# Optimization experiments

Measured on AMD Instinct MI355X. Metric: run time of the kernel, lower is better.

The kernel has to match this reference:

```python
import jax, jax.numpy as jnp
import numpy as np

B, S, H = 32, 512, 768
NHEAD, DH = 8, 96          # 8 heads * 96 = 768
E = 4096                   # edges per sample
NC = 2
NEG = -1e9
EPS = 1e-5


def _p(k, shape, scale=0.02):
    return scale * jax.random.normal(k, shape, dtype=jnp.float32)


def setup_inputs() -> dict:
    key = jax.random.key(0)
    ks = jax.random.split(key, 24)
    z = lambda *s: jnp.zeros(s, jnp.float32)
    return {
        "diff_encoded": jax.random.normal(ks[0], (B, S, H), jnp.float32),
        "msg_encoded": jax.random.normal(ks[1], (B, S, H), jnp.float32),
        "msg_mask": jnp.ones((B, S), jnp.int32),
        "edge_index_diff": jax.random.randint(ks[2], (B, 2, E), 0, S),
        "edge_index_msg": jax.random.randint(ks[3], (B, 2, E), 0, S),
        # GATv2Conv(heads=1): lin_l (source/message), lin_r (target), att vector, output bias
        "gat_wl": _p(ks[4], (H, H)), "gat_bl": z(H),
        "gat_wr": _p(ks[5], (H, H)), "gat_br": z(H),
        "gat_att": _p(ks[6], (H,)), "gat_bias": z(H),
        # cross MultiheadAttention
        "wq": _p(ks[7], (H, H)), "bq": z(H),
        "wk": _p(ks[8], (H, H)), "bk": z(H),
        "wv": _p(ks[9], (H, H)), "bv": z(H),
        "wo": _p(ks[10], (H, H)), "bo": z(H),
        # LayerNorm + MLP head
        "ln_g": jnp.ones((H,), jnp.float32), "ln_b": z(H),
        "fc0_w": _p(ks[11], (H, 512)), "fc0_b": z(512),
        "fc1_w": _p(ks[12], (512, 128)), "fc1_b": z(128),
        "fc2_w": _p(ks[13], (128, NC)), "fc2_b": z(NC),
    }


def _gat_single(x, edges, wl, bl, wr, br, att, bias):
    # GATv2Conv, heads=1, add_self_loops=True. x: [N,H], edges: [2,E] (src, dst).
    N = x.shape[0]
    src, dst = edges[0], edges[1]
    valid = (src < N) & (dst < N)            # clip_edge_index, as a mask
    src = jnp.where(valid, src, 0)
    dst = jnp.where(valid, dst, 0)
    loop = jnp.arange(N, dtype=src.dtype)    # PyG adds self loops
    src_a = jnp.concatenate([src, loop])
    dst_a = jnp.concatenate([dst, loop])
    valid_a = jnp.concatenate([valid, jnp.ones((N,), bool)])
    xl = x @ wl + bl                          # source / message transform
    xr = x @ wr + br                          # target transform
    e = jax.nn.leaky_relu(xl[src_a] + xr[dst_a], 0.2) @ att   # [E+N]
    e = jnp.where(valid_a, e, NEG)
    emax = jax.ops.segment_max(e, dst_a, num_segments=N)
    p = jnp.exp(e - emax[dst_a]) * valid_a.astype(x.dtype)
    denom = jax.ops.segment_sum(p, dst_a, num_segments=N)
    alpha = p / denom[dst_a]
    out = jax.ops.segment_sum(alpha[:, None] * xl[src_a], dst_a, num_segments=N)
    return out + bias


_gat = jax.vmap(_gat_single, in_axes=(0, 0) + (None,) * 6)


def _layernorm(x, g, b):
    mu = jnp.mean(x, -1, keepdims=True)
    var = jnp.mean(jnp.square(x - mu), -1, keepdims=True)
    return (x - mu) * jax.lax.rsqrt(var + EPS) * g + b


def reference(diff_encoded, msg_encoded, msg_mask, edge_index_diff, edge_index_msg,
              gat_wl, gat_bl, gat_wr, gat_br, gat_att, gat_bias,
              wq, bq, wk, bk, wv, bv, wo, bo, ln_g, ln_b,
              fc0_w, fc0_b, fc1_w, fc1_b, fc2_w, fc2_b):
    diff_g = _gat(diff_encoded, edge_index_diff, gat_wl, gat_bl, gat_wr, gat_br, gat_att, gat_bias) + diff_encoded
    msg_g = _gat(msg_encoded, edge_index_msg, gat_wl, gat_bl, gat_wr, gat_br, gat_att, gat_bias) + msg_encoded
    # cross attention: query=diff_g, key/value=msg_g, key_padding_mask = (msg_mask == 0)
    q = (diff_g @ wq + bq).reshape(B, S, NHEAD, DH)
    k = (msg_g @ wk + bk).reshape(B, S, NHEAD, DH)
    v = (msg_g @ wv + bv).reshape(B, S, NHEAD, DH)
    scores = jnp.einsum("bqhd,bkhd->bhqk", q, k) / jnp.sqrt(jnp.float32(DH))
    scores = jnp.where((msg_mask == 0)[:, None, None, :], NEG, scores)
    attn = jax.nn.softmax(scores, axis=-1)
    ctx = jnp.einsum("bhqk,bkhd->bqhd", attn, v).reshape(B, S, H) @ wo + bo
    fused = _layernorm(ctx + diff_g, ln_g, ln_b)
    x = fused[:, 0, :]                                  # CLS token
    x = jax.nn.relu(x @ fc0_w + fc0_b)                  # dropout = identity (eval)
    x = jax.nn.relu(x @ fc1_w + fc1_b)
    return x @ fc2_w + fc2_b
```

## Files before the change

### kernel.cpp

```cpp
#include <hip/hip_runtime.h>
#include <hip/hip_bf16.h>
#include <math.h>

#define BB 32
#define SS 512
#define HH 768
#define NHEADC 8
#define DHC 96
#define EE 4096
#define NCC 2
#define CAPC 128
#define CAP2 32
#define GSL 36
#define XRS 1536
#define NEGV -1000000000.0f
#define EPSV 1e-5f

#define PREP_CVT  12288
#define PREP_WT   2304
#define PREP_BIAS 3
#define PREP_CNT  512
#define PREP_TOT  (PREP_CVT + PREP_WT + PREP_BIAS + PREP_CNT)

typedef __hip_bfloat16 bf16;
typedef __bf16 bf16x8 __attribute__((ext_vector_type(8)));
typedef float f32x4 __attribute__((ext_vector_type(4)));

static __device__ inline unsigned short f2bf_u(float f) {
  __hip_bfloat16 h = __float2bfloat16(f);
  return *(unsigned short*)&h;
}
static __device__ inline float bfu(unsigned short u) {
  return __uint_as_float(((unsigned int)u) << 16);
}
static __device__ inline float bf2f(bf16 h) { return __bfloat162float(h); }

static __device__ inline void gload16(const void* g, void* l) {
  __builtin_amdgcn_global_load_lds(
      (const __attribute__((address_space(1))) void*)g,
      (__attribute__((address_space(3))) void*)l, 16, 0, 0);
}

__global__ __launch_bounds__(256) void k_prep(
    const float* __restrict__ msg_enc, bf16* __restrict__ Abf,
    const float* __restrict__ gat_wl, const float* __restrict__ gat_wr,
    const float* __restrict__ wk, const float* __restrict__ wv,
    bf16* __restrict__ wtA, bf16* __restrict__ wtB,
    const float* __restrict__ gat_bl, const float* __restrict__ gat_br,
    const float* __restrict__ bk, const float* __restrict__ bv,
    float* __restrict__ biasA, float* __restrict__ biasB,
    const int* __restrict__ e_msg, const int* __restrict__ e_diff,
    int* __restrict__ cnt, int* __restrict__ dcnt, int* __restrict__ dsrc)
{
  int blk = blockIdx.x, tid = threadIdx.x;
  if (blk < PREP_CVT) {
    int i = (blk * 256 + tid) * 4;
    float4 v = *(const float4*)(msg_enc + i);
    ushort4 o;
    o.x = f2bf_u(v.x); o.y = f2bf_u(v.y); o.z = f2bf_u(v.z); o.w = f2bf_u(v.w);
    *(ushort4*)((unsigned short*)Abf + i) = o;
    return;
  }
  blk -= PREP_CVT;
  if (blk < PREP_WT) {
    int z = blk / 576, rr = blk - z * 576;
    int bx = rr % 24, by = rr / 24;
    const float* w; bf16* o;
    switch (z) {
      case 0: w = gat_wl; o = wtA; break;
      case 1: w = gat_wr; o = wtA + (size_t)HH * HH; break;
      case 2: w = wk;     o = wtB; break;
      default: w = wv;    o = wtB + (size_t)HH * HH; break;
    }
    __shared__ float t[32][33];
    int n0 = bx * 32, k0 = by * 32;
    int x = tid & 31, y = tid >> 5;
    for (int yy = y; yy < 32; yy += 8)
      t[yy][x] = w[(size_t)(k0 + yy) * HH + n0 + x];
    __syncthreads();
    for (int yy = y; yy < 32; yy += 8)
      o[(size_t)(n0 + yy) * HH + k0 + x] = __float2bfloat16(t[x][yy]);
    return;
  }
  blk -= PREP_WT;
  if (blk < PREP_BIAS) {
    int t = blk * 256 + tid;
    if (t < HH) {
      biasA[t] = gat_bl[t]; biasA[HH + t] = gat_br[t];
      biasB[t] = bk[t];     biasB[HH + t] = bv[t];
    }
    return;
  }
  blk -= PREP_BIAS;
  {
    int i = blk * 256 + tid;
    if (i >= BB * EE) return;
    int b = i / EE, j = i - b * EE;
    int s = e_msg[b * 2 * EE + j], d = e_msg[b * 2 * EE + EE + j];
    if (s >= 0 && s < SS && d >= 0 && d < SS)
      atomicAdd(&cnt[b * SS + d], 1);
    int s2 = e_diff[b * 2 * EE + j], d2 = e_diff[b * 2 * EE + EE + j];
    if (s2 >= 0 && s2 < SS && d2 == 0) {
      int pos = atomicAdd(&dcnt[b], 1);
      if (pos < CAPC) dsrc[b * CAPC + pos] = s2;
    }
    if (j == 0) {
      int pos = atomicAdd(&dcnt[b], 1);
      if (pos < CAPC) dsrc[b * CAPC + pos] = 0;
    }
  }
}

template <typename OT>
__global__ __launch_bounds__(256) void k_gemm(
    const bf16* __restrict__ A, const bf16* __restrict__ Bt,
    const float* __restrict__ bias, OT* __restrict__ C,
    int M, int N, int K, int ldc)
{
  __shared__ __align__(16) bf16 As0[128 * 32];
  __shared__ __align__(16) bf16 As1[128 * 32];
  __shared__ __align__(16) bf16 Bs0[128 * 32];
  __shared__ __align__(16) bf16 Bs1[128 * 32];
  const int tid = threadIdx.x;
  const int wv = tid >> 6, lane = tid & 63;
  const int bm = blockIdx.x * 128, bn = blockIdx.y * 128;
  const int wm = (wv & 1) * 64, wn = (wv >> 1) * 64;
  const int m16 = lane & 15, half = lane >> 4;
  f32x4 acc[4][4];
  #pragma unroll
  for (int i = 0; i < 4; ++i)
    #pragma unroll
    for (int j = 0; j < 4; ++j) acc[i][j] = (f32x4){0.f, 0.f, 0.f, 0.f};

  const int c0 = tid, c1 = tid + 256;
  const int r0 = c0 >> 2, o0 = (c0 & 3) * 8;
  const int r1 = c1 >> 2, o1 = (c1 & 3) * 8;
  const size_t aB0 = (size_t)(bm + r0) * K + o0;
  const size_t aB1 = (size_t)(bm + r1) * K + o1;
  const size_t bB0 = (size_t)(bn + r0) * K + o0;
  const size_t bB1 = (size_t)(bn + r1) * K + o1;

  for (int k0 = 0; k0 < K; k0 += 64) {
    __syncthreads();
    gload16(A + aB0 + k0, As0 + (size_t)c0 * 8);
    gload16(A + aB1 + k0, As0 + (size_t)c1 * 8);
    gload16(A + aB0 + k0 + 32, As1 + (size_t)c0 * 8);
    gload16(A + aB1 + k0 + 32, As1 + (size_t)c1 * 8);
    gload16(Bt + bB0 + k0, Bs0 + (size_t)c0 * 8);
    gload16(Bt + bB1 + k0, Bs0 + (size_t)c1 * 8);
    gload16(Bt + bB0 + k0 + 32, Bs1 + (size_t)c0 * 8);
    gload16(Bt + bB1 + k0 + 32, Bs1 + (size_t)c1 * 8);
    __syncthreads();
    #pragma unroll
    for (int ks = 0; ks < 2; ++ks) {
      const bf16* Ah = ks ? As1 : As0;
      const bf16* Bh = ks ? Bs1 : Bs0;
      bf16x8 af[4], bfv[4];
      #pragma unroll
      for (int t = 0; t < 4; ++t) {
        af[t]  = *(const bf16x8*)(Ah + (wm + t * 16 + m16) * 32 + half * 8);
        bfv[t] = *(const bf16x8*)(Bh + (wn + t * 16 + m16) * 32 + half * 8);
      }
      #pragma unroll
      for (int i = 0; i < 4; ++i)
        #pragma unroll
        for (int j = 0; j < 4; ++j)
          acc[i][j] = __builtin_amdgcn_mfma_f32_16x16x32_bf16(af[i], bfv[j], acc[i][j], 0, 0, 0);
    }
  }
  #pragma unroll
  for (int i = 0; i < 4; ++i) {
    #pragma unroll
    for (int j = 0; j < 4; ++j) {
      int col = bn + wn + j * 16 + m16;
      float bv = bias ? bias[col] : 0.f;
      #pragma unroll
      for (int r = 0; r < 4; ++r) {
        int row = bm + wm + i * 16 + half * 4 + r;
        float v = acc[i][j][r] + bv;
        if constexpr (sizeof(OT) == 2)
          C[(size_t)row * ldc + col] = (OT)__float2bfloat16(v);
        else
          C[(size_t)row * ldc + col] = v;
      }
    }
  }
}

__global__ __launch_bounds__(512) void k_scan(const int* __restrict__ cnt,
                                              int* __restrict__ offs,
                                              int* __restrict__ cursor) {
  __shared__ int tmp[SS];
  int b = blockIdx.x, t = threadIdx.x;
  int x = cnt[b * SS + t];
  tmp[t] = x;
  __syncthreads();
  for (int off = 1; off < SS; off <<= 1) {
    int u = (t >= off) ? tmp[t - off] : 0;
    __syncthreads();
    tmp[t] += u;
    __syncthreads();
  }
  int ex = tmp[t] - x;
  offs[b * SS + t] = ex;
  cursor[b * SS + t] = ex;
}

__global__ void k_scatter(const int* __restrict__ e_msg, int* __restrict__ cursor,
                          int* __restrict__ binned) {
  int i = blockIdx.x * blockDim.x + threadIdx.x;
  if (i >= BB * EE) return;
  int b = i / EE, j = i - b * EE;
  int s = e_msg[b * 2 * EE + j], d = e_msg[b * 2 * EE + EE + j];
  if (s >= 0 && s < SS && d >= 0 && d < SS) {
    int pos = atomicAdd(&cursor[b * SS + d], 1);
    binned[(size_t)b * EE + pos] = s;
  }
}

__global__ __launch_bounds__(256) void k_gat_fused(
    const int* __restrict__ binned, const int* __restrict__ offs,
    const int* __restrict__ cnt, const bf16* __restrict__ xlr,
    const float* __restrict__ att, const float* __restrict__ gbias,
    const float* __restrict__ resid, bf16* __restrict__ out)
{
  int g = blockIdx.x * 4 + (threadIdx.x >> 6);
  int lane = threadIdx.x & 63;
  int b = g / SS, d = g - b * SS;
  int base = offs[b * SS + d], n = cnt[b * SS + d];
  const int* bin = binned + (size_t)b * EE + base;
  float av[12];
  {
    const float4* a4 = (const float4*)att;
    #pragma unroll
    for (int r = 0; r < 3; ++r) {
      float4 t = a4[lane + 64 * r];
      av[4*r] = t.x; av[4*r+1] = t.y; av[4*r+2] = t.z; av[4*r+3] = t.w;
    }
  }
  float xr[12];
  {
    const ushort4* p = (const ushort4*)(xlr + ((size_t)b * SS + d) * XRS + HH);
    #pragma unroll
    for (int r = 0; r < 3; ++r) {
      ushort4 v = p[lane + 64 * r];
      xr[4*r] = bfu(v.x); xr[4*r+1] = bfu(v.y); xr[4*r+2] = bfu(v.z); xr[4*r+3] = bfu(v.w);
    }
  }
  float m = -3.0e38f, l = 0.f;
  float acc[12] = {};
  for (int i = -1; i < n; ++i) {
    int s = (i < 0) ? d : bin[i];
    float xs[12];
    const ushort4* p = (const ushort4*)(xlr + ((size_t)b * SS + s) * XRS);
    #pragma unroll
    for (int r = 0; r < 3; ++r) {
      ushort4 v = p[lane + 64 * r];
      xs[4*r] = bfu(v.x); xs[4*r+1] = bfu(v.y); xs[4*r+2] = bfu(v.z); xs[4*r+3] = bfu(v.w);
    }
    float e = 0.f;
    #pragma unroll
    for (int k = 0; k < 12; ++k) {
      float t = xs[k] + xr[k];
      t = t > 0.f ? t : 0.2f * t;
      e += t * av[k];
    }
    #pragma unroll
    for (int off = 32; off > 0; off >>= 1) e += __shfl_xor(e, off);
    float mn = fmaxf(m, e);
    float so = __expf(m - mn);
    float w  = __expf(e - mn);
    l = l * so + w;
    #pragma unroll
    for (int k = 0; k < 12; ++k) acc[k] = acc[k] * so + w * xs[k];
    m = mn;
  }
  float inv = 1.f / l;
  size_t o = ((size_t)b * SS + d) * HH;
  const float4* gb4 = (const float4*)gbias;
  const float4* rs4 = (const float4*)(resid + o);
  ushort4* out4 = (ushort4*)(out + o);
  #pragma unroll
  for (int r = 0; r < 3; ++r) {
    int c = lane + 64 * r;
    float4 gg = gb4[c], rr = rs4[c];
    ushort4 ov;
    ov.x = f2bf_u(acc[4*r+0] * inv + gg.x + rr.x);
    ov.y = f2bf_u(acc[4*r+1] * inv + gg.y + rr.y);
    ov.z = f2bf_u(acc[4*r+2] * inv + gg.z + rr.z);
    ov.w = f2bf_u(acc[4*r+3] * inv + gg.w + rr.w);
    out4[c] = ov;
  }
}

__global__ __launch_bounds__(192) void k_gather_diff(
    const int* __restrict__ dcnt, const int* __restrict__ dsrc,
    const float* __restrict__ diff_enc, bf16* __restrict__ G)
{
  int b = blockIdx.y, jj = blockIdx.x;
  int n = min(dcnt[b], CAP2);
  int t = threadIdx.x;
  size_t orow = ((size_t)b * GSL + jj) * HH;
  ushort4 o = {0, 0, 0, 0};
  if (jj < n || jj == CAP2) {
    int s = (jj == CAP2) ? 0 : dsrc[b * CAPC + jj];
    float4 v = ((const float4*)(diff_enc + ((size_t)b * SS + s) * HH))[t];
    o.x = f2bf_u(v.x); o.y = f2bf_u(v.y); o.z = f2bf_u(v.z); o.w = f2bf_u(v.w);
  }
  *(ushort4*)((unsigned short*)G + orow + t * 4) = o;
}

__global__ __launch_bounds__(256) void k_diff_gat0(
    const int* __restrict__ dcnt, const float* __restrict__ GD,
    const float* __restrict__ att, const float* __restrict__ gbias,
    const float* __restrict__ diff_enc, float* __restrict__ dg0)
{
  int b = blockIdx.x;
  int n = min(dcnt[b], CAP2);
  __shared__ float ee[CAP2];
  __shared__ float al[CAP2];
  __shared__ float xr0s[HH];
  int wave = threadIdx.x >> 6, lane = threadIdx.x & 63;
  for (int h = threadIdx.x; h < HH; h += 256)
    xr0s[h] = GD[((size_t)b * GSL + CAP2) * XRS + HH + h];
  __syncthreads();
  for (int jj = wave; jj < n; jj += 4) {
    const float* px = GD + ((size_t)b * GSL + jj) * XRS;
    float part = 0.f;
    #pragma unroll
    for (int r = 0; r < HH / 64; ++r) {
      int h = lane + 64 * r;
      float t = px[h] + xr0s[h];
      t = t > 0.f ? t : 0.2f * t;
      part += t * att[h];
    }
    #pragma unroll
    for (int off = 32; off > 0; off >>= 1) part += __shfl_xor(part, off);
    if (lane == 0) ee[jj] = part;
  }
  __syncthreads();
  if (threadIdx.x == 0) {
    float m = -3.0e38f;
    for (int i = 0; i < n; ++i) m = fmaxf(m, ee[i]);
    float ssum = 0.f;
    for (int i = 0; i < n; ++i) ssum += expf(ee[i] - m);
    float inv = 1.f / ssum;
    for (int i = 0; i < n; ++i) al[i] = expf(ee[i] - m) * inv;
  }
  __syncthreads();
  for (int h = threadIdx.x; h < HH; h += 256) {
    float acc = 0.f;
    for (int i = 0; i < n; ++i) acc += al[i] * GD[((size_t)b * GSL + i) * XRS + h];
    dg0[b * HH + h] = acc + gbias[h] + diff_enc[(size_t)b * SS * HH + h];
  }
}

__global__ __launch_bounds__(256) void k_colmat(
    const float* __restrict__ in, const float* __restrict__ w,
    const float* __restrict__ bias, const float* __restrict__ extra,
    float* __restrict__ outp, int Kd, int Nd, long in_stride, int relu)
{
  int b = blockIdx.y, n0 = blockIdx.x * 64;
  int tid = threadIdx.x, wv = tid >> 6, lane = tid & 63;
  __shared__ float xs[HH];
  __shared__ float red[4][64];
  const float* src = in + (size_t)b * in_stride;
  for (int k = tid; k < Kd; k += 256) xs[k] = src[k];
  __syncthreads();
  int h = n0 + lane;
  int kpw = Kd >> 2;
  int kb = wv * kpw;
  float acc = 0.f;
  for (int k = 0; k < kpw; k += 8) {
    #pragma unroll
    for (int u = 0; u < 8; ++u) {
      int kk = kb + k + u;
      acc += xs[kk] * w[(size_t)kk * Nd + h];
    }
  }
  red[wv][lane] = acc;
  __syncthreads();
  if (tid < 64) {
    float s = red[0][tid] + red[1][tid] + red[2][tid] + red[3][tid] + bias[n0 + tid];
    if (extra) s += extra[(size_t)b * Nd + n0 + tid];
    if (relu) s = fmaxf(s, 0.f);
    outp[(size_t)b * Nd + n0 + tid] = s;
  }
}

__global__ __launch_bounds__(256) void k_ln(
    const float* __restrict__ xin, const float* __restrict__ g,
    const float* __restrict__ bta, float* __restrict__ yout)
{
  int b = blockIdx.x, tid = threadIdx.x;
  __shared__ float red[4], redq[4];
  float v0 = xin[b * HH + tid];
  float v1 = xin[b * HH + tid + 256];
  float v2 = xin[b * HH + tid + 512];
  float sum = v0 + v1 + v2;
  float sq = v0 * v0 + v1 * v1 + v2 * v2;
  #pragma unroll
  for (int off = 32; off > 0; off >>= 1) { sum += __shfl_xor(sum, off); sq += __shfl_xor(sq, off); }
  int wv = tid >> 6, lane = tid & 63;
  if (lane == 0) { red[wv] = sum; redq[wv] = sq; }
  __syncthreads();
  sum = red[0] + red[1] + red[2] + red[3];
  sq = redq[0] + redq[1] + redq[2] + redq[3];
  float mu = sum / HH;
  float var = sq / HH - mu * mu;
  float scl = rsqrtf(var + EPSV);
  yout[b * HH + tid]       = (v0 - mu) * scl * g[tid]       + bta[tid];
  yout[b * HH + tid + 256] = (v1 - mu) * scl * g[tid + 256] + bta[tid + 256];
  yout[b * HH + tid + 512] = (v2 - mu) * scl * g[tid + 512] + bta[tid + 512];
}

__global__ __launch_bounds__(256) void k_fc12(
    const float* __restrict__ a0g, const float* __restrict__ fc1w,
    const float* __restrict__ fc1b, const float* __restrict__ fc2w,
    const float* __restrict__ fc2b, float* __restrict__ out)
{
  int b = blockIdx.x, tid = threadIdx.x;
  __shared__ float a0s[512];
  __shared__ float a1s[128];
  __shared__ float r1[2][128];
  for (int k = tid; k < 512; k += 256) a0s[k] = a0g[b * 512 + k];
  __syncthreads();
  int o = tid & 127, hf = tid >> 7;
  int kb = hf * 256;
  float acc = 0.f;
  for (int k = 0; k < 256; k += 8) {
    #pragma unroll
    for (int u = 0; u < 8; ++u) {
      int kk = kb + k + u;
      acc += a0s[kk] * fc1w[(size_t)kk * 128 + o];
    }
  }
  r1[hf][o] = acc;
  __syncthreads();
  if (tid < 128) a1s[tid] = fmaxf(r1[0][tid] + r1[1][tid] + fc1b[tid], 0.f);
  __syncthreads();
  if (tid < 128) {
    int oo = tid >> 6, l = tid & 63;
    float p = a1s[l] * fc2w[l * 2 + oo] + a1s[l + 64] * fc2w[(l + 64) * 2 + oo];
    #pragma unroll
    for (int off = 32; off > 0; off >>= 1) p += __shfl_xor(p, off);
    if (l == 0) out[b * NCC + oo] = p + fc2b[oo];
  }
}

__global__ __launch_bounds__(512) void k_attn(
    const float* __restrict__ q0, const bf16* __restrict__ kvb,
    const int* __restrict__ mask, float* __restrict__ ctx)
{
  int b = blockIdx.x / NHEADC, hd = blockIdx.x % NHEADC;
  __shared__ float qs[DHC];
  __shared__ float sc[SS];
  __shared__ float redm[8];
  __shared__ float reds[8];
  __shared__ float pr4[4][DHC];
  int tid = threadIdx.x;
  if (tid < DHC) qs[tid] = q0[b * HH + hd * DHC + tid];
  __syncthreads();
  const float scale = 0.10206207261596575f;
  {
    int s = tid;
    const int4* pk4 = (const int4*)(kvb + ((size_t)b * SS + s) * XRS + hd * DHC);
    float acc = 0.f;
    #pragma unroll
    for (int c = 0; c < 12; ++c) {
      int4 raw = pk4[c];
      const unsigned short* u = (const unsigned short*)&raw;
      #pragma unroll
      for (int j = 0; j < 8; ++j) acc += qs[c * 8 + j] * bfu(u[j]);
    }
    sc[s] = (mask[b * SS + s] != 0) ? acc * scale : NEGV;
  }
  __syncthreads();
  int wave = tid >> 6, lane = tid & 63;
  float m = sc[tid];
  #pragma unroll
  for (int off = 32; off > 0; off >>= 1) m = fmaxf(m, __shfl_xor(m, off));
  if (lane == 0) redm[wave] = m;
  __syncthreads();
  m = redm[0];
  #pragma unroll
  for (int i = 1; i < 8; ++i) m = fmaxf(m, redm[i]);
  float p0 = expf(sc[tid] - m);
  float ssum = p0;
  #pragma unroll
  for (int off = 32; off > 0; off >>= 1) ssum += __shfl_xor(ssum, off);
  if (lane == 0) reds[wave] = ssum;
  __syncthreads();
  ssum = reds[0] + reds[1] + reds[2] + reds[3] + reds[4] + reds[5] + reds[6] + reds[7];
  float inv = 1.f / ssum;
  sc[tid] = p0 * inv;
  __syncthreads();
  {
    int hs = tid >> 7, d = tid & 127;
    if (d < DHC) {
      const bf16* pv = kvb + ((size_t)b * SS + hs * 128) * XRS + HH + hd * DHC + d;
      float acc = 0.f;
      for (int s = 0; s < 128; s += 8) {
        #pragma unroll
        for (int u = 0; u < 8; ++u)
          acc += sc[hs * 128 + s + u] * bf2f(pv[(size_t)(s + u) * XRS]);
      }
      pr4[hs][d] = acc;
    }
  }
  __syncthreads();
  if (tid < DHC)
    ctx[b * HH + hd * DHC + tid] = pr4[0][tid] + pr4[1][tid] + pr4[2][tid] + pr4[3][tid];
}

extern "C" void kernel_launch(void* const* d_in, const int* in_sizes, int n_in,
                              void* d_out, int out_size, void* d_ws, size_t ws_size,
                              hipStream_t stream) {
  const float* diff_enc = (const float*)d_in[0];
  const float* msg_enc  = (const float*)d_in[1];
  const int*   msg_mask = (const int*)d_in[2];
  const int*   e_diff   = (const int*)d_in[3];
  const int*   e_msg    = (const int*)d_in[4];
  const float* gat_wl   = (const float*)d_in[5];
  const float* gat_bl   = (const float*)d_in[6];
  const float* gat_wr   = (const float*)d_in[7];
  const float* gat_br   = (const float*)d_in[8];
  const float* gat_att  = (const float*)d_in[9];
  const float* gat_bias = (const float*)d_in[10];
  const float* wq = (const float*)d_in[11];
  const float* bq = (const float*)d_in[12];
  const float* wk = (const float*)d_in[13];
  const float* bk = (const float*)d_in[14];
  const float* wv = (const float*)d_in[15];
  const float* bv = (const float*)d_in[16];
  const float* wo = (const float*)d_in[17];
  const float* bo = (const float*)d_in[18];
  const float* ln_g = (const float*)d_in[19];
  const float* ln_b = (const float*)d_in[20];
  const float* fc0w = (const float*)d_in[21];
  const float* fc0b = (const float*)d_in[22];
  const float* fc1w = (const float*)d_in[23];
  const float* fc1b = (const float*)d_in[24];
  const float* fc2w = (const float*)d_in[25];
  const float* fc2b = (const float*)d_in[26];
  float* out = (float*)d_out;

  char* ws = (char*)d_ws;
  size_t off = 0;
  auto alloc = [&](size_t bytes) -> void* {
    void* p = (void*)(ws + off);
    off += (bytes + 255) & ~(size_t)255;
    return p;
  };
  bf16* Abf    = (bf16*)alloc((size_t)BB * SS * HH * 2);
  bf16* xlr    = (bf16*)alloc((size_t)BB * SS * XRS * 2);
  bf16* kv     = (bf16*)alloc((size_t)BB * SS * XRS * 2);
  bf16* mg     = (bf16*)alloc((size_t)BB * SS * HH * 2);
  bf16* wtA    = (bf16*)alloc((size_t)2 * HH * HH * 2);
  bf16* wtB    = (bf16*)alloc((size_t)2 * HH * HH * 2);
  float* biasA = (float*)alloc((size_t)XRS * 4);
  float* biasB = (float*)alloc((size_t)XRS * 4);
  int*   cnt   = (int*)alloc((size_t)BB * SS * 4);
  int*   offs  = (int*)alloc((size_t)BB * SS * 4);
  int*   cursor= (int*)alloc((size_t)BB * SS * 4);
  int*   binned= (int*)alloc((size_t)BB * EE * 4);
  bf16*  G     = (bf16*)alloc((size_t)BB * GSL * HH * 2);
  float* GD    = (float*)alloc((size_t)BB * GSL * XRS * 4);
  int*   dcnt  = (int*)alloc((size_t)BB * 4);
  int*   dsrc  = (int*)alloc((size_t)BB * CAPC * 4);
  float* dg0   = (float*)alloc((size_t)BB * HH * 4);
  float* q0    = (float*)alloc((size_t)BB * HH * 4);
  float* ctx   = (float*)alloc((size_t)BB * HH * 4);
  float* fpre  = (float*)alloc((size_t)BB * HH * 4);
  float* fnrm  = (float*)alloc((size_t)BB * HH * 4);
  float* a0g   = (float*)alloc((size_t)BB * 512 * 4);

  hipMemsetAsync(cnt, 0, (size_t)BB * SS * 4, stream);
  hipMemsetAsync(dcnt, 0, (size_t)BB * 4, stream);

  k_prep<<<PREP_TOT, 256, 0, stream>>>(msg_enc, Abf, gat_wl, gat_wr, wk, wv,
                                       wtA, wtB, gat_bl, gat_br, bk, bv,
                                       biasA, biasB, e_msg, e_diff,
                                       cnt, dcnt, dsrc);
  k_scan<<<BB, SS, 0, stream>>>(cnt, offs, cursor);
  k_scatter<<<(BB * EE + 255) / 256, 256, 0, stream>>>(e_msg, cursor, binned);

  dim3 gBlk(256), gGridA((BB * SS) / 128, XRS / 128);
  k_gemm<bf16><<<gGridA, gBlk, 0, stream>>>(Abf, wtA, biasA, xlr,
                                            BB * SS, XRS, HH, XRS);
  k_gat_fused<<<(BB * SS) / 4, 256, 0, stream>>>(binned, offs, cnt, xlr,
                                                 gat_att, gat_bias, msg_enc, mg);
  k_gemm<bf16><<<gGridA, gBlk, 0, stream>>>(mg, wtB, biasB, kv,
                                            BB * SS, XRS, HH, XRS);
  {
    dim3 gg(GSL, BB);
    k_gather_diff<<<gg, 192, 0, stream>>>(dcnt, dsrc, diff_enc, G);
    dim3 gGridD((BB * GSL) / 128, XRS / 128);
    k_gemm<float><<<gGridD, gBlk, 0, stream>>>(G, wtA, biasA, GD,
                                               BB * GSL, XRS, HH, XRS);
  }
  k_diff_gat0<<<BB, 256, 0, stream>>>(dcnt, GD, gat_att, gat_bias, diff_enc, dg0);
  {
    dim3 g(HH / 64, BB);
    k_colmat<<<g, 256, 0, stream>>>(dg0, wq, bq, nullptr, q0, HH, HH, HH, 0);
  }
  k_attn<<<BB * NHEADC, 512, 0, stream>>>(q0, kv, msg_mask, ctx);
  {
    dim3 g(HH / 64, BB);
    k_colmat<<<g, 256, 0, stream>>>(ctx, wo, bo, dg0, fpre, HH, HH, HH, 0);
  }
  k_ln<<<BB, 256, 0, stream>>>(fpre, ln_g, ln_b, fnrm);
  {
    dim3 g(512 / 64, BB);
    k_colmat<<<g, 256, 0, stream>>>(fnrm, fc0w, fc0b, nullptr, a0g, HH, 512, HH, 1);
  }
  k_fc12<<<BB, 256, 0, stream>>>(a0g, fc1w, fc1b, fc2w, fc2b, out);
}
```

Baseline: 447.7 us.

## Swizzle GEMM LDS layout, remap GAT blocks per XCD, read bf16 residual

The GEMM now XOR-swizzles the 16-byte chunk column in shared memory on both the global-to-LDS store and the fragment load, to cut LDS bank conflicts. The fused GAT kernel remaps block IDs so that each XCD processes four contiguous batches, keeping xlr and binned data local to one L2. It also reads the residual from the existing bf16 copy of msg_encoded instead of the fp32 original, halving that read traffic. The price is that the residual add is now rounded to bf16 first, which slightly changes numerics.

Result: no change. 441.1 us (-1.5%).

```diff
diff --git a/kernel.cpp b/kernel.cpp
--- a/kernel.cpp
+++ b/kernel.cpp
@@ -126,6 +126,7 @@
   const int bm = blockIdx.x * 128, bn = blockIdx.y * 128;
   const int wm = (wv & 1) * 64, wn = (wv >> 1) * 64;
   const int m16 = lane & 15, half = lane >> 4;
+  const int swz = (half ^ (m16 & 3)) * 8;
   f32x4 acc[4][4];
   #pragma unroll
   for (int i = 0; i < 4; ++i)
@@ -133,8 +134,8 @@
     for (int j = 0; j < 4; ++j) acc[i][j] = (f32x4){0.f, 0.f, 0.f, 0.f};
 
   const int c0 = tid, c1 = tid + 256;
-  const int r0 = c0 >> 2, o0 = (c0 & 3) * 8;
-  const int r1 = c1 >> 2, o1 = (c1 & 3) * 8;
+  const int r0 = c0 >> 2, o0 = (((c0 & 3) ^ ((c0 >> 2) & 3))) * 8;
+  const int r1 = c1 >> 2, o1 = (((c1 & 3) ^ ((c1 >> 2) & 3))) * 8;
   const size_t aB0 = (size_t)(bm + r0) * K + o0;
   const size_t aB1 = (size_t)(bm + r1) * K + o1;
   const size_t bB0 = (size_t)(bn + r0) * K + o0;
@@ -158,8 +159,8 @@
       bf16x8 af[4], bfv[4];
       #pragma unroll
       for (int t = 0; t < 4; ++t) {
-        af[t]  = *(const bf16x8*)(Ah + (wm + t * 16 + m16) * 32 + half * 8);
-        bfv[t] = *(const bf16x8*)(Bh + (wn + t * 16 + m16) * 32 + half * 8);
+        af[t]  = *(const bf16x8*)(Ah + (wm + t * 16 + m16) * 32 + swz);
+        bfv[t] = *(const bf16x8*)(Bh + (wn + t * 16 + m16) * 32 + swz);
       }
       #pragma unroll
       for (int i = 0; i < 4; ++i)
@@ -222,11 +223,15 @@
     const int* __restrict__ binned, const int* __restrict__ offs,
     const int* __restrict__ cnt, const bf16* __restrict__ xlr,
     const float* __restrict__ att, const float* __restrict__ gbias,
-    const float* __restrict__ resid, bf16* __restrict__ out)
-{
-  int g = blockIdx.x * 4 + (threadIdx.x >> 6);
+    const bf16* __restrict__ resid, bf16* __restrict__ out)
+{
+  int bid = blockIdx.x;
+  int xcd = bid & 7, idx = bid >> 3;
+  int batch = xcd * 4 + (idx >> 7);
+  int within = idx & 127;
   int lane = threadIdx.x & 63;
-  int b = g / SS, d = g - b * SS;
+  int b = batch;
+  int d = within * 4 + (threadIdx.x >> 6);
   int base = offs[b * SS + d], n = cnt[b * SS + d];
   const int* bin = binned + (size_t)b * EE + base;
   float av[12];
@@ -278,17 +283,18 @@
   float inv = 1.f / l;
   size_t o = ((size_t)b * SS + d) * HH;
   const float4* gb4 = (const float4*)gbias;
-  const float4* rs4 = (const float4*)(resid + o);
+  const ushort4* rs4 = (const ushort4*)(resid + o);
   ushort4* out4 = (ushort4*)(out + o);
   #pragma unroll
   for (int r = 0; r < 3; ++r) {
     int c = lane + 64 * r;
-    float4 gg = gb4[c], rr = rs4[c];
+    float4 gg = gb4[c];
+    ushort4 rr = rs4[c];
     ushort4 ov;
-    ov.x = f2bf_u(acc[4*r+0] * inv + gg.x + rr.x);
-    ov.y = f2bf_u(acc[4*r+1] * inv + gg.y + rr.y);
-    ov.z = f2bf_u(acc[4*r+2] * inv + gg.z + rr.z);
-    ov.w = f2bf_u(acc[4*r+3] * inv + gg.w + rr.w);
+    ov.x = f2bf_u(acc[4*r+0] * inv + gg.x + bfu(rr.x));
+    ov.y = f2bf_u(acc[4*r+1] * inv + gg.y + bfu(rr.y));
+    ov.z = f2bf_u(acc[4*r+2] * inv + gg.z + bfu(rr.z));
+    ov.w = f2bf_u(acc[4*r+3] * inv + gg.w + bfu(rr.w));
     out4[c] = ov;
   }
 }
@@ -589,7 +595,7 @@
   k_gemm<bf16><<<gGridA, gBlk, 0, stream>>>(Abf, wtA, biasA, xlr,
                                             BB * SS, XRS, HH, XRS);
   k_gat_fused<<<(BB * SS) / 4, 256, 0, stream>>>(binned, offs, cnt, xlr,
-                                                 gat_att, gat_bias, msg_enc, mg);
+                                                 gat_att, gat_bias, Abf, mg);
   k_gemm<bf16><<<gGridA, gBlk, 0, stream>>>(mg, wtB, biasB, kv,
                                             BB * SS, XRS, HH, XRS);
   {
```
